# Kernel tuning notes

Hardware: AMD Instinct MI355X
Metric: run time of the kernel (lower is better)

## Reference

```python
import jax, jax.numpy as jnp
import numpy as np

KERNEL = 3  # kernel_size from init_kwargs


def _unfold(x, k):
    """torch.nn.functional.unfold with padding=k//2, stride=1.
    Returns [b, c*k*k, h*w] with torch's ordering: index = c*(k*k) + kh*k + kw.
    """
    b, c, h, w = x.shape
    p = k // 2
    xp = jnp.pad(x, ((0, 0), (0, 0), (p, p), (p, p)))
    # fixed k*k = 9 slices (small static loop, not a data-dim loop)
    cols = jnp.stack(
        [xp[:, :, i:i + h, j:j + w] for i in range(k) for j in range(k)],
        axis=2,
    )  # [b, c, k*k, h, w]
    return cols.reshape(b, c * k * k, h * w)


def setup_inputs() -> dict:
    key = jax.random.key(0)
    k1, k2 = jax.random.split(key)
    x = jax.random.normal(k1, (8, 64, 128, 128), dtype=jnp.float32)
    # memory parameter: torch.rand -> uniform [0, 1), shape [c*k*k, out_channels]
    memory = jax.random.uniform(k2, (64 * KERNEL * KERNEL, 128), dtype=jnp.float32)
    return {"x": x, "memory": memory}


def reference(x, memory):
    b, c, h, w = x.shape
    cols = _unfold(x, KERNEL)                 # [b, c*k*k, h*w]
    cols = jax.nn.softmax(cols, axis=1)       # softmax over unfolded patch dim
    out = jnp.einsum('ki,bkl->bil', memory, cols)  # [b, out_ch, h*w]
    return out.reshape(b, memory.shape[1], h, w)
```

## Files before the change

kernel.cpp:

```cpp
#include <hip/hip_runtime.h>
#include <stdint.h>


#define Cn 64
#define Hn 128
#define Wn 128
#define OC 128
#define HW (Hn * Wn)

typedef __attribute__((ext_vector_type(8))) short bf16x8_t;
typedef __attribute__((ext_vector_type(4))) float f32x4_t;
typedef __attribute__((ext_vector_type(16))) float f32x16_t;

__device__ inline unsigned short f2bf(float f) {
    union { float f; uint32_t u; } v; v.f = f;
    uint32_t u = v.u;
    u += 0x7fffu + ((u >> 16) & 1u);
    return (unsigned short)(u >> 16);
}
__device__ inline float bf2f(unsigned short h) {
    union { uint32_t u; float f; } v; v.u = ((uint32_t)h) << 16;
    return v.f;
}

__global__ void prep_b2(const float* __restrict__ mem, uint4* __restrict__ Bt2,
                        uint4* __restrict__ ones) {
    if (blockIdx.x == 36) {
        if (threadIdx.x < 8)
            ones[threadIdx.x] = make_uint4(0x3F803F80u, 0x3F803F80u, 0x3F803F80u, 0x3F803F80u);
        return;
    }
    int u = blockIdx.x * 256 + threadIdx.x;
    int n = u & 127;
    int cid = u >> 7;
    int hi = cid & 1;
    int kc = cid >> 1;
    int q = kc >> 2, cblk = kc & 3;
    unsigned short h8[8];
#pragma unroll
    for (int j = 0; j < 8; j++) {
        int c = cblk * 16 + hi * 8 + j;
        h8[j] = f2bf(mem[(c * 9 + q) * OC + n]);
    }
    Bt2[cid * 128 + n] = *(const uint4*)h8;
}

__global__ __launch_bounds__(256) void exp_tr2(const float* __restrict__ x,
                                               uint4* __restrict__ Etu,
                                               float* __restrict__ S) {
    __shared__ float lf[64][130];
    int bid = blockIdx.x;
    int b = bid >> 7, h = bid & 127;
    int t = threadIdx.x;
    int wv = t >> 6, lane = t & 63;

    const float* xr = x + (size_t)b * Cn * HW + h * Wn;
#pragma unroll
    for (int i = 0; i < 16; i++) {
        int c = i * 4 + wv;
        float2 v = *(const float2*)(xr + (size_t)c * HW + lane * 2);
        lf[c][2 * lane + 0] = __expf(v.x);
        lf[c][2 * lane + 1] = __expf(v.y);
    }
    __syncthreads();

    int w = t >> 1, ch0 = (t & 1) * 32;
    unsigned short us[32];
    float s = 0.f;
#pragma unroll
    for (int j = 0; j < 32; j++) {
        unsigned short hb = f2bf(lf[ch0 + j][w]);
        us[j] = hb;
        s += bf2f(hb);
    }
    size_t pix = (size_t)(b * Hn + h) * Wn + w;
    uint4* dst = Etu + pix * 8 + (t & 1) * 4;
    const uint4* srcv = (const uint4*)us;
    dst[0] = srcv[0]; dst[1] = srcv[1]; dst[2] = srcv[2]; dst[3] = srcv[3];

    s += __shfl_xor(s, 1);
    if ((t & 1) == 0) S[pix] = s;
}

__global__ __launch_bounds__(512, 2) void conv2(const uint4* __restrict__ Etu,
                                                const uint4* __restrict__ Bt2,
                                                const float* __restrict__ S,
                                                const uint4* __restrict__ ones,
                                                float* __restrict__ out) {
    __shared__ __align__(16) uint4 EtL[324 * 8];
    __shared__ float Sh[324];
    __shared__ __align__(16) float Zt[256];

    int bid = blockIdx.x;
    int b = bid >> 6;
    int ty = (bid >> 3) & 7, tx = bid & 7;
    int h0 = ty * 16, w0 = tx * 16;
    int t = threadIdx.x;

    const uint4* Etb = Etu + (size_t)b * HW * 8;
#pragma unroll
    for (int i = 0; i < 6; i++) {
        int qd = i * 512 + t;
        if (qd < 2592) {
            int p = qd >> 3, sslot = qd & 7;
            int py = p / 18, px = p - py * 18;
            int gy = h0 - 1 + py, gx = w0 - 1 + px;
            bool in = (gy >= 0) & (gy < Hn) & (gx >= 0) & (gx < Wn);
            int g = sslot ^ (p & 7);
            const uint4* src = in ? (Etb + ((size_t)(gy * Wn + gx)) * 8 + g)
                                  : (ones + g);
            EtL[p * 8 + sslot] = *src;
        }
    }
    if (t < 324) {
        int py = t / 18, px = t - py * 18;
        int gy = h0 - 1 + py, gx = w0 - 1 + px;
        bool in = (gy >= 0) & (gy < Hn) & (gx >= 0) & (gx < Wn);
        Sh[t] = in ? S[(size_t)b * HW + gy * Wn + gx] : 64.0f;
    }
    __syncthreads();

    if (t < 256) {
        int zy = t >> 4, zx = t & 15;
        float z = 0.f;
#pragma unroll
        for (int dy = 0; dy < 3; dy++)
#pragma unroll
            for (int dx = 0; dx < 3; dx++)
                z += Sh[(zy + dy) * 18 + (zx + dx)];
        Zt[t] = 1.0f / z;
    }
    __syncthreads();

    int lane = t & 63, wv = t >> 6;
    int row = lane & 31, hi = lane >> 5;
    int py0 = wv * 2 + (row >> 4);
    int px0 = row & 15;

    f32x16_t acc[4];
#pragma unroll
    for (int nb = 0; nb < 4; nb++)
#pragma unroll
        for (int r = 0; r < 16; r++) acc[nb][r] = 0.f;

    bf16x8_t Af[2];
    bf16x8_t Bf[2][4];

    auto loadK = [&](int kc, bf16x8_t& Ad, bf16x8_t* Bd) {
        int q = kc >> 2, cblk = kc & 3;
        int kh = q / 3, kw = q - kh * 3;
        int pix = (py0 + kh) * 18 + (px0 + kw);
        int g = cblk * 2 + hi;
        Ad = *(const bf16x8_t*)&EtL[pix * 8 + (g ^ (pix & 7))];
        const uint4* bp = Bt2 + (size_t)(kc * 2 + hi) * 128 + row;
#pragma unroll
        for (int nb = 0; nb < 4; nb++)
            Bd[nb] = *(const bf16x8_t*)(bp + nb * 32);
    };

    loadK(0, Af[0], Bf[0]);
#pragma unroll 2
    for (int kc = 0; kc < 36; kc++) {
        int cur = kc & 1, nxt = cur ^ 1;
        if (kc + 1 < 36) loadK(kc + 1, Af[nxt], Bf[nxt]);
#pragma unroll
        for (int nb = 0; nb < 4; nb++)
            acc[nb] = __builtin_amdgcn_mfma_f32_32x32x16_bf16(Af[cur], Bf[cur][nb], acc[nb], 0, 0, 0);
    }

#pragma unroll
    for (int g4 = 0; g4 < 4; g4++) {
        int rowbase = g4 * 8 + hi * 4;
        int p = wv * 32 + rowbase;
        int yy = p >> 4, xx = p & 15;
        f32x4_t zi = *(const f32x4_t*)&Zt[p];
#pragma unroll
        for (int nb = 0; nb < 4; nb++) {
            int n = nb * 32 + row;
            f32x4_t v;
            v.x = acc[nb][g4 * 4 + 0] * zi.x;
            v.y = acc[nb][g4 * 4 + 1] * zi.y;
            v.z = acc[nb][g4 * 4 + 2] * zi.z;
            v.w = acc[nb][g4 * 4 + 3] * zi.w;
            *(f32x4_t*)(out + ((size_t)(b * OC + n) * HW + (h0 + yy) * Wn + (w0 + xx))) = v;
        }
    }
}

extern "C" void kernel_launch(void* const* d_in, const int* in_sizes, int n_in,
                              void* d_out, int out_size, void* d_ws, size_t ws_size,
                              hipStream_t stream) {
    const float* x = (const float*)d_in[0];
    const float* mem = (const float*)d_in[1];
    float* out = (float*)d_out;
    char* ws = (char*)d_ws;

    uint4* Etu = (uint4*)ws;
    float* S = (float*)(ws + 16777216);
    uint4* Bt2 = (uint4*)(ws + 17301504);
    uint4* ones = (uint4*)(ws + 17448960);

    prep_b2<<<37, 256, 0, stream>>>(mem, Bt2, ones);
    exp_tr2<<<1024, 256, 0, stream>>>(x, Etu, S);
    conv2<<<512, 512, 0, stream>>>(Etu, Bt2, S, ones, out);
}
```

Before: 123.4 us.

## Shrink conv tiles, swap MFMA operands, pack bf16 in exp transpose

The exp/transpose kernel now converts to bf16 before staging in shared memory, which halves LDS traffic. It also remaps threads so each wave handles contiguous pixels, with the channel-half sum reduced through shared memory. The conv kernel uses 8x16 pixel tiles with 256 threads and 1024 blocks, aiming for more blocks and occupancy. MFMA operands are swapped so weights form the A side and pixels the B side, which lets each lane store output rows coalesced along width. In exchange, halo overhead per tile rises (180 loaded pixels for 128 outputs) and the stores become scalar per lane.

Result: no change. 124.7 us (+1.0%).

```diff
diff --git a/kernel.cpp b/kernel.cpp
--- a/kernel.cpp
+++ b/kernel.cpp
@@ -45,10 +45,11 @@
     Bt2[cid * 128 + n] = *(const uint4*)h8;
 }
 
-__global__ __launch_bounds__(256) void exp_tr2(const float* __restrict__ x,
+__global__ __launch_bounds__(256) void exp_tr3(const float* __restrict__ x,
                                                uint4* __restrict__ Etu,
                                                float* __restrict__ S) {
-    __shared__ float lf[64][130];
+    __shared__ uint32_t lu[64 * 68];
+    __shared__ float Spart[256];
     int bid = blockIdx.x;
     int b = bid >> 7, h = bid & 127;
     int t = threadIdx.x;
@@ -59,60 +60,63 @@
     for (int i = 0; i < 16; i++) {
         int c = i * 4 + wv;
         float2 v = *(const float2*)(xr + (size_t)c * HW + lane * 2);
-        lf[c][2 * lane + 0] = __expf(v.x);
-        lf[c][2 * lane + 1] = __expf(v.y);
-    }
-    __syncthreads();
-
-    int w = t >> 1, ch0 = (t & 1) * 32;
+        uint32_t pk = (uint32_t)f2bf(__expf(v.x)) | ((uint32_t)f2bf(__expf(v.y)) << 16);
+        lu[c * 68 + lane] = pk;
+    }
+    __syncthreads();
+
+    const unsigned short* Lp = (const unsigned short*)lu;
+    int w = t & 127, ch0 = (t >> 7) * 32;
     unsigned short us[32];
     float s = 0.f;
 #pragma unroll
     for (int j = 0; j < 32; j++) {
-        unsigned short hb = f2bf(lf[ch0 + j][w]);
+        unsigned short hb = Lp[(ch0 + j) * 136 + w];
         us[j] = hb;
         s += bf2f(hb);
     }
     size_t pix = (size_t)(b * Hn + h) * Wn + w;
-    uint4* dst = Etu + pix * 8 + (t & 1) * 4;
+    uint4* dst = Etu + pix * 8 + (t >> 7) * 4;
     const uint4* srcv = (const uint4*)us;
     dst[0] = srcv[0]; dst[1] = srcv[1]; dst[2] = srcv[2]; dst[3] = srcv[3];
 
-    s += __shfl_xor(s, 1);
-    if ((t & 1) == 0) S[pix] = s;
-}
-
-__global__ __launch_bounds__(512, 2) void conv2(const uint4* __restrict__ Etu,
+    Spart[t] = s;
+    __syncthreads();
+    if (t < 128)
+        S[pix] = Spart[t] + Spart[t + 128];
+}
+
+__global__ __launch_bounds__(256, 4) void conv3(const uint4* __restrict__ Etu,
                                                 const uint4* __restrict__ Bt2,
                                                 const float* __restrict__ S,
                                                 const uint4* __restrict__ ones,
                                                 float* __restrict__ out) {
-    __shared__ __align__(16) uint4 EtL[324 * 8];
-    __shared__ float Sh[324];
-    __shared__ __align__(16) float Zt[256];
+    __shared__ __align__(16) uint4 EtL[180 * 8];
+    __shared__ float Sh[180];
+    __shared__ float Zt[128];
 
     int bid = blockIdx.x;
-    int b = bid >> 6;
-    int ty = (bid >> 3) & 7, tx = bid & 7;
-    int h0 = ty * 16, w0 = tx * 16;
+    int b = bid >> 7;
+    int ty = (bid >> 3) & 15, tx = bid & 7;
+    int h0 = ty * 8, w0 = tx * 16;
     int t = threadIdx.x;
 
     const uint4* Etb = Etu + (size_t)b * HW * 8;
 #pragma unroll
     for (int i = 0; i < 6; i++) {
-        int qd = i * 512 + t;
-        if (qd < 2592) {
-            int p = qd >> 3, sslot = qd & 7;
+        int qd = i * 256 + t;
+        if (qd < 1440) {
+            int p = qd >> 3, slot = qd & 7;
             int py = p / 18, px = p - py * 18;
             int gy = h0 - 1 + py, gx = w0 - 1 + px;
             bool in = (gy >= 0) & (gy < Hn) & (gx >= 0) & (gx < Wn);
-            int g = sslot ^ (p & 7);
+            int g = slot ^ (p & 7);
             const uint4* src = in ? (Etb + ((size_t)(gy * Wn + gx)) * 8 + g)
                                   : (ones + g);
-            EtL[p * 8 + sslot] = *src;
+            EtL[p * 8 + slot] = *src;
         }
     }
-    if (t < 324) {
+    if (t < 180) {
         int py = t / 18, px = t - py * 18;
         int gy = h0 - 1 + py, gx = w0 - 1 + px;
         bool in = (gy >= 0) & (gy < Hn) & (gx >= 0) & (gx < Wn);
@@ -120,7 +124,7 @@
     }
     __syncthreads();
 
-    if (t < 256) {
+    if (t < 128) {
         int zy = t >> 4, zx = t & 15;
         float z = 0.f;
 #pragma unroll
@@ -133,56 +137,55 @@
     __syncthreads();
 
     int lane = t & 63, wv = t >> 6;
-    int row = lane & 31, hi = lane >> 5;
-    int py0 = wv * 2 + (row >> 4);
-    int px0 = row & 15;
+    int l31 = lane & 31, hi = lane >> 5;
+    int y0 = wv * 2 + (l31 >> 4);
+    int x0 = l31 & 15;
 
     f32x16_t acc[4];
 #pragma unroll
-    for (int nb = 0; nb < 4; nb++)
-#pragma unroll
-        for (int r = 0; r < 16; r++) acc[nb][r] = 0.f;
-
-    bf16x8_t Af[2];
-    bf16x8_t Bf[2][4];
-
-    auto loadK = [&](int kc, bf16x8_t& Ad, bf16x8_t* Bd) {
+    for (int g = 0; g < 4; g++)
+#pragma unroll
+        for (int r = 0; r < 16; r++) acc[g][r] = 0.f;
+
+    bf16x8_t Wf[2][4], Ef[2];
+
+    auto loadW = [&](int kc, bf16x8_t* Wd) {
+        const uint4* bp = Bt2 + (size_t)((kc * 2 + hi) * 128 + l31);
+#pragma unroll
+        for (int g = 0; g < 4; g++)
+            Wd[g] = *(const bf16x8_t*)(bp + g * 32);
+    };
+    auto loadE = [&](int kc, bf16x8_t& Ed) {
         int q = kc >> 2, cblk = kc & 3;
         int kh = q / 3, kw = q - kh * 3;
-        int pix = (py0 + kh) * 18 + (px0 + kw);
+        int pix = (y0 + kh) * 18 + (x0 + kw);
         int g = cblk * 2 + hi;
-        Ad = *(const bf16x8_t*)&EtL[pix * 8 + (g ^ (pix & 7))];
-        const uint4* bp = Bt2 + (size_t)(kc * 2 + hi) * 128 + row;
-#pragma unroll
-        for (int nb = 0; nb < 4; nb++)
-            Bd[nb] = *(const bf16x8_t*)(bp + nb * 32);
+        Ed = *(const bf16x8_t*)&EtL[pix * 8 + (g ^ (pix & 7))];
     };
 
-    loadK(0, Af[0], Bf[0]);
-#pragma unroll 2
+    loadW(0, Wf[0]);
+    loadE(0, Ef[0]);
+#pragma unroll
     for (int kc = 0; kc < 36; kc++) {
         int cur = kc & 1, nxt = cur ^ 1;
-        if (kc + 1 < 36) loadK(kc + 1, Af[nxt], Bf[nxt]);
-#pragma unroll
-        for (int nb = 0; nb < 4; nb++)
-            acc[nb] = __builtin_amdgcn_mfma_f32_32x32x16_bf16(Af[cur], Bf[cur][nb], acc[nb], 0, 0, 0);
-    }
-
-#pragma unroll
-    for (int g4 = 0; g4 < 4; g4++) {
-        int rowbase = g4 * 8 + hi * 4;
-        int p = wv * 32 + rowbase;
-        int yy = p >> 4, xx = p & 15;
-        f32x4_t zi = *(const f32x4_t*)&Zt[p];
-#pragma unroll
-        for (int nb = 0; nb < 4; nb++) {
-            int n = nb * 32 + row;
-            f32x4_t v;
-            v.x = acc[nb][g4 * 4 + 0] * zi.x;
-            v.y = acc[nb][g4 * 4 + 1] * zi.y;
-            v.z = acc[nb][g4 * 4 + 2] * zi.z;
-            v.w = acc[nb][g4 * 4 + 3] * zi.w;
-            *(f32x4_t*)(out + ((size_t)(b * OC + n) * HW + (h0 + yy) * Wn + (w0 + xx))) = v;
+        if (kc + 1 < 36) {
+            loadW(kc + 1, Wf[nxt]);
+            loadE(kc + 1, Ef[nxt]);
+        }
+#pragma unroll
+        for (int g = 0; g < 4; g++)
+            acc[g] = __builtin_amdgcn_mfma_f32_32x32x16_bf16(Wf[cur][g], Ef[cur], acc[g], 0, 0, 0);
+    }
+
+    float zi = Zt[wv * 32 + l31];
+    float* obase = out + (size_t)b * OC * HW + (h0 + y0) * Wn + (w0 + x0)
+                 + (size_t)(4 * hi) * HW;
+#pragma unroll
+    for (int g = 0; g < 4; g++) {
+#pragma unroll
+        for (int r = 0; r < 16; r++) {
+            int nrel = g * 32 + (r & 3) + 8 * (r >> 2);
+            obase[(size_t)nrel * HW] = acc[g][r] * zi;
         }
     }
 }
@@ -201,6 +204,6 @@
     uint4* ones = (uint4*)(ws + 17448960);
 
     prep_b2<<<37, 256, 0, stream>>>(mem, Bt2, ones);
-    exp_tr2<<<1024, 256, 0, stream>>>(x, Etu, S);
-    conv2<<<512, 512, 0, stream>>>(Etu, Bt2, S, ones, out);
-}
+    exp_tr3<<<1024, 256, 0, stream>>>(x, Etu, S);
+    conv3<<<1024, 256, 0, stream>>>(Etu, Bt2, S, ones, out);
+}
```
